# Optimization experiments

Hardware: AMD Instinct MI355X
Metric: run time of the kernel (lower is better)

## Reference

```python
import jax, jax.numpy as jnp
import numpy as np

NEG_SLOPE = 0.2

def _gatv2_layer(x, src, tgt, Wl, Wr, att, bias, num_nodes, heads, ch):
    # x: [N, Fin]; src/tgt: [E] (self loops already included)
    xl = (x @ Wl).reshape(num_nodes, heads, ch)  # source transform [N,H,C]
    xr = (x @ Wr).reshape(num_nodes, heads, ch)  # target transform [N,H,C]
    m = xl[src] + xr[tgt]                        # [E,H,C]
    m = jnp.where(m > 0, m, NEG_SLOPE * m)       # LeakyReLU
    e = jnp.einsum('ehc,hc->eh', m, att)         # attention logits [E,H]
    # softmax over incoming edges of each target node (numerically stable)
    e_max = jax.ops.segment_max(e, tgt, num_segments=num_nodes)
    e_max = jnp.where(jnp.isfinite(e_max), e_max, 0.0)
    alpha = jnp.exp(e - e_max[tgt])              # [E,H]
    denom = jax.ops.segment_sum(alpha, tgt, num_segments=num_nodes)
    alpha = alpha / (denom[tgt] + 1e-16)
    out = jax.ops.segment_sum(alpha[:, :, None] * xl[src], tgt, num_segments=num_nodes)  # [N,H,C]
    return out.mean(axis=1) + bias               # concat=False -> mean over heads, then bias


def setup_inputs() -> dict:
    key = jax.random.key(0)
    ks = jax.random.split(key, 12)
    N, E = 50000, 800000
    IN, HID, H = 128, 64, 2
    features = jax.random.normal(ks[0], (N, IN), dtype=jnp.float32)
    edge_index = jax.random.randint(ks[1], (2, E), 0, N, dtype=jnp.int64)
    s = 0.1
    return {
        'features': features,
        'edge_index': edge_index,
        'Wl1': jax.random.normal(ks[2], (IN, H * HID), dtype=jnp.float32) * s,
        'Wr1': jax.random.normal(ks[3], (IN, H * HID), dtype=jnp.float32) * s,
        'att1': jax.random.normal(ks[4], (H, HID), dtype=jnp.float32) * s,
        'b1': jnp.zeros((HID,), dtype=jnp.float32),
        'Wl2': jax.random.normal(ks[5], (HID, H * HID), dtype=jnp.float32) * s,
        'Wr2': jax.random.normal(ks[6], (HID, H * HID), dtype=jnp.float32) * s,
        'att2': jax.random.normal(ks[7], (H, HID), dtype=jnp.float32) * s,
        'b2': jnp.zeros((HID,), dtype=jnp.float32),
    }


def reference(features, edge_index, Wl1, Wr1, att1, b1, Wl2, Wr2, att2, b2):
    N = features.shape[0]
    H, HID = att1.shape
    # PyG GATv2Conv default add_self_loops=True
    loop = jnp.arange(N, dtype=edge_index.dtype)
    src = jnp.concatenate([edge_index[0], loop])
    tgt = jnp.concatenate([edge_index[1], loop])
    h = _gatv2_layer(features, src, tgt, Wl1, Wr1, att1, b1, N, H, HID)
    h = jax.nn.relu(h)
    out = _gatv2_layer(h, src, tgt, Wl2, Wr2, att2, b2, N, H, HID)
    return out  # node_mask in original is None
```

## Files before the change

kernel.cpp:

```cpp
#include <hip/hip_runtime.h>
#include <hip/hip_bf16.h>
#include <math.h>


#define HEADS 2
#define CH 64
#define FDIM (HEADS * CH)
#define CAP 48
#define HBLK 3328

typedef _Float16 f16_t;
typedef _Float16 f16x4 __attribute__((ext_vector_type(4)));
typedef _Float16 f16x8 __attribute__((ext_vector_type(8)));
typedef float f32x4 __attribute__((ext_vector_type(4)));


__global__ __launch_bounds__(256)
void init_kernel(const float* __restrict__ Wl1, const float* __restrict__ Wr1,
                 const float* __restrict__ Wl2, const float* __restrict__ Wr2,
                 f16_t* __restrict__ fl1, f16_t* __restrict__ fr1,
                 f16_t* __restrict__ fl2, f16_t* __restrict__ fr2,
                 int* __restrict__ cnt, int N) {
    int bx = blockIdx.x;
    if (bx < 4) {
        const float* W; f16_t* F; int K;
        switch (bx) {
            case 0:  W = Wl1; F = fl1; K = 128; break;
            case 1:  W = Wr1; F = fr1; K = 128; break;
            case 2:  W = Wl2; F = fl2; K = 64;  break;
            default: W = Wr2; F = fr2; K = 64;  break;
        }
        int S = K >> 5;
        int total = 8 * S * 64;
        for (int idx = threadIdx.x; idx < total; idx += blockDim.x) {
            int l  = idx & 63;
            int ts = idx >> 6;
            int s  = ts % S;
            int t  = ts / S;
            int n  = t * 16 + (l & 15);
            int k0 = s * 32 + (l >> 4) * 8;
            f16x8 v;
            #pragma unroll
            for (int j = 0; j < 8; ++j) v[j] = (f16_t)W[(size_t)(k0 + j) * 128 + n];
            *(f16x8*)(F + (size_t)idx * 8) = v;
        }
    } else {
        int n4 = (N + 3) >> 2;
        int stride = (gridDim.x - 4) * blockDim.x;
        for (int i = (bx - 4) * blockDim.x + threadIdx.x; i < n4; i += stride) {
            int i0 = i * 4;
            if (i0 + 3 < N) *(int4*)(cnt + i0) = make_int4(0, 0, 0, 0);
            else for (int k = 0; k < 4 && i0 + k < N; ++k) cnt[i0 + k] = 0;
        }
    }
}


__device__ __forceinline__ unsigned int pack_bf16x2(float x, float y) {
    __hip_bfloat16 lo = __float2bfloat16(x);
    __hip_bfloat16 hi = __float2bfloat16(y);
    unsigned short ulo = *reinterpret_cast<unsigned short*>(&lo);
    unsigned short uhi = *reinterpret_cast<unsigned short*>(&hi);
    return ((unsigned int)uhi << 16) | ulo;
}

__device__ __forceinline__
void gemm_body(const float* __restrict__ X,
               const f16_t* __restrict__ FL, const f16_t* __restrict__ FR,
               unsigned int* __restrict__ Y0b, float* __restrict__ Y1,
               int N, int K, int gblk, float* lds_f) {
    f16_t* Af = (f16_t*)lds_f;
    int tid  = threadIdx.x;
    int lane = tid & 63;
    int wave = tid >> 6;
    int row0 = gblk * 32;
    int S = K >> 5;

    {
        int r  = tid >> 3;
        int m  = r & 15;
        int g  = r >> 4;
        int gr = row0 + r;
        int kc = (tid & 7) * (K >> 3);
        const float* xp = X + (size_t)gr * K + kc;
        f16_t* areg = Af + g * (16 * K);
        for (int c = 0; c < (K >> 3); c += 4) {
            float4 xv = make_float4(0.f, 0.f, 0.f, 0.f);
            if (gr < N) xv = *(const float4*)(xp + c);
            int k = kc + c;
            int s = k >> 5;
            int lanei = ((k >> 3) & 3) * 16 + m;
            int j = k & 7;
            f16x4 h;
            h[0] = (f16_t)xv.x; h[1] = (f16_t)xv.y;
            h[2] = (f16_t)xv.z; h[3] = (f16_t)xv.w;
            *(f16x4*)(areg + ((s * 64 + lanei) * 8 + j)) = h;
        }
    }
    __syncthreads();

    int rg  = wave >> 1;
    int mat = wave & 1;
    const f16_t* F = mat ? FR : FL;

    f32x4 acc[8];
    #pragma unroll
    for (int t = 0; t < 8; ++t) acc[t] = (f32x4){0.f, 0.f, 0.f, 0.f};

    const f16_t* aw = Af + rg * (16 * K);
    for (int s = 0; s < S; ++s) {
        f16x8 a = *(const f16x8*)(aw + (s * 64 + lane) * 8);
        #pragma unroll
        for (int t = 0; t < 8; ++t) {
            f16x8 b = *(const f16x8*)(F + ((size_t)(t * S + s) * 64 + lane) * 8);
            acc[t] = __builtin_amdgcn_mfma_f32_16x16x32_f16(a, b, acc[t], 0, 0, 0);
        }
    }
    __syncthreads();

    float* ew = lds_f + wave * (16 * 68);
    int mrow = (lane >> 4) * 4;
    int ccol = lane & 15;
    int rr = lane & 15;
    int ch = lane >> 4;
    int gr2 = row0 + rg * 16 + rr;

    #pragma unroll
    for (int h = 0; h < 2; ++h) {
        #pragma unroll
        for (int tt = 0; tt < 4; ++tt)
            #pragma unroll
            for (int r = 0; r < 4; ++r)
                ew[(mrow + r) * 68 + tt * 16 + ccol] = acc[h * 4 + tt][r];
        __syncthreads();
        if (gr2 < N) {
            const float* src = ew + rr * 68 + ch * 16;
            if (mat == 0) {
                uint4 o0, o1;
                o0.x = pack_bf16x2(src[0],  src[1]);
                o0.y = pack_bf16x2(src[2],  src[3]);
                o0.z = pack_bf16x2(src[4],  src[5]);
                o0.w = pack_bf16x2(src[6],  src[7]);
                o1.x = pack_bf16x2(src[8],  src[9]);
                o1.y = pack_bf16x2(src[10], src[11]);
                o1.z = pack_bf16x2(src[12], src[13]);
                o1.w = pack_bf16x2(src[14], src[15]);
                unsigned int* dst = Y0b + (size_t)gr2 * (FDIM / 2) + h * 32 + ch * 8;
                *(uint4*)dst       = o0;
                *(uint4*)(dst + 4) = o1;
            } else {
                float* dst = Y1 + (size_t)gr2 * FDIM + h * 64 + ch * 16;
                #pragma unroll
                for (int q = 0; q < 4; ++q)
                    *(float4*)(dst + q * 4) = *(const float4*)(src + q * 4);
            }
        }
        __syncthreads();
    }
}

__global__ __launch_bounds__(256)
void fused_scatter_gemm_kernel(const float* __restrict__ X,
                               const f16_t* __restrict__ FL,
                               const f16_t* __restrict__ FR,
                               unsigned int* __restrict__ Y0b,
                               float* __restrict__ Y1,
                               int N, int K,
                               const int* __restrict__ ei, int* __restrict__ cnt,
                               int* __restrict__ ssrc, int E) {
    __shared__ float lds_f[4352];

    if (blockIdx.x < HBLK) {
        int vb   = blockIdx.x;
        int part = vb & 7;
        int blk  = vb >> 3;
        int nblk = HBLK >> 3;
        int lo = (int)(((long long)N * part) >> 3);
        int hi = (int)(((long long)N * (part + 1)) >> 3);
        int stride = nblk * blockDim.x;
        int G = E >> 2;
        for (int g = blk * blockDim.x + threadIdx.x; g < G; g += stride) {
            int4 t4 = *(const int4*)(ei + E + g * 4);
            if (t4.x >= lo && t4.x < hi) {
                int k = atomicAdd(&cnt[t4.x], 1);
                if (k < CAP) ssrc[t4.x * CAP + k] = ei[g * 4 + 0];
            }
            if (t4.y >= lo && t4.y < hi) {
                int k = atomicAdd(&cnt[t4.y], 1);
                if (k < CAP) ssrc[t4.y * CAP + k] = ei[g * 4 + 1];
            }
            if (t4.z >= lo && t4.z < hi) {
                int k = atomicAdd(&cnt[t4.z], 1);
                if (k < CAP) ssrc[t4.z * CAP + k] = ei[g * 4 + 2];
            }
            if (t4.w >= lo && t4.w < hi) {
                int k = atomicAdd(&cnt[t4.w], 1);
                if (k < CAP) ssrc[t4.w * CAP + k] = ei[g * 4 + 3];
            }
        }
        for (int e = (G << 2) + blk * blockDim.x + threadIdx.x; e < E; e += stride) {
            int t = ei[E + e];
            if (t >= lo && t < hi) {
                int k = atomicAdd(&cnt[t], 1);
                if (k < CAP) ssrc[t * CAP + k] = ei[e];
            }
        }
        for (int n = lo + blk * blockDim.x + threadIdx.x; n < hi; n += stride) {
            int k = atomicAdd(&cnt[n], 1);
            if (k < CAP) ssrc[n * CAP + k] = n;
        }
        return;
    }

    gemm_body(X, FL, FR, Y0b, Y1, N, K, blockIdx.x - HBLK, lds_f);
}

__global__ __launch_bounds__(256)
void gemm_kernel(const float* __restrict__ X,
                 const f16_t* __restrict__ FL, const f16_t* __restrict__ FR,
                 unsigned int* __restrict__ Y0b, float* __restrict__ Y1,
                 int N, int K) {
    __shared__ float lds_f[4352];
    gemm_body(X, FL, FR, Y0b, Y1, N, K, blockIdx.x, lds_f);
}


__device__ __forceinline__ void unpack_bf16x2(unsigned int u, float& x, float& y) {
    x = __uint_as_float(u << 16);
    y = __uint_as_float(u & 0xFFFF0000u);
}

__device__ __forceinline__ float2 lrelu2(float2 t) {
    t.x = fmaxf(t.x, 0.2f * t.x);
    t.y = fmaxf(t.y, 0.2f * t.y);
    return t;
}

__global__ __launch_bounds__(256)
void agg_kernel(const unsigned int* __restrict__ xlb, const float* __restrict__ xr,
                const int* __restrict__ cnt, const int* __restrict__ ssrc,
                const float* __restrict__ att, const float* __restrict__ bias,
                float* __restrict__ out, int N, int do_relu) {
    int node = blockIdx.x * 4 + (threadIdx.x >> 6);
    int lane = threadIdx.x & 63;
    if (node >= N) return;

    float2 xr2 = *(const float2*)(xr + (size_t)node * FDIM + 2 * lane);
    float2 a2  = *(const float2*)(att + 2 * lane);

    int beg = node * CAP;
    int deg = cnt[node];
    deg = min(deg, CAP);
    int end = beg + deg;

    float l = 0.f;
    float2 acc = make_float2(0.f, 0.f);

    bool b0 = (lane & 1) != 0;
    bool b1 = (lane & 2) != 0;
    bool b2 = (lane & 4) != 0;
    int base = lane & 32;

    int i = beg;
    int n8 = beg + (deg & ~7);
    for (; i < n8; i += 8) {
        int s0 = ssrc[i + 0];
        int s1 = ssrc[i + 1];
        int s2 = ssrc[i + 2];
        int s3 = ssrc[i + 3];
        int s4 = ssrc[i + 4];
        int s5 = ssrc[i + 5];
        int s6 = ssrc[i + 6];
        int s7 = ssrc[i + 7];
        unsigned int u0 = xlb[(size_t)s0 * (FDIM / 2) + lane];
        unsigned int u1 = xlb[(size_t)s1 * (FDIM / 2) + lane];
        unsigned int u2 = xlb[(size_t)s2 * (FDIM / 2) + lane];
        unsigned int u3 = xlb[(size_t)s3 * (FDIM / 2) + lane];
        unsigned int u4 = xlb[(size_t)s4 * (FDIM / 2) + lane];
        unsigned int u5 = xlb[(size_t)s5 * (FDIM / 2) + lane];
        unsigned int u6 = xlb[(size_t)s6 * (FDIM / 2) + lane];
        unsigned int u7 = xlb[(size_t)s7 * (FDIM / 2) + lane];
        float2 v0, v1, v2, v3, v4, v5, v6, v7;
        unpack_bf16x2(u0, v0.x, v0.y);
        unpack_bf16x2(u1, v1.x, v1.y);
        unpack_bf16x2(u2, v2.x, v2.y);
        unpack_bf16x2(u3, v3.x, v3.y);
        unpack_bf16x2(u4, v4.x, v4.y);
        unpack_bf16x2(u5, v5.x, v5.y);
        unpack_bf16x2(u6, v6.x, v6.y);
        unpack_bf16x2(u7, v7.x, v7.y);

        float2 t0 = lrelu2(make_float2(v0.x + xr2.x, v0.y + xr2.y));
        float2 t1 = lrelu2(make_float2(v1.x + xr2.x, v1.y + xr2.y));
        float2 t2 = lrelu2(make_float2(v2.x + xr2.x, v2.y + xr2.y));
        float2 t3 = lrelu2(make_float2(v3.x + xr2.x, v3.y + xr2.y));
        float2 t4 = lrelu2(make_float2(v4.x + xr2.x, v4.y + xr2.y));
        float2 t5 = lrelu2(make_float2(v5.x + xr2.x, v5.y + xr2.y));
        float2 t6 = lrelu2(make_float2(v6.x + xr2.x, v6.y + xr2.y));
        float2 t7 = lrelu2(make_float2(v7.x + xr2.x, v7.y + xr2.y));
        float p0 = fmaf(t0.x, a2.x, t0.y * a2.y);
        float p1 = fmaf(t1.x, a2.x, t1.y * a2.y);
        float p2 = fmaf(t2.x, a2.x, t2.y * a2.y);
        float p3 = fmaf(t3.x, a2.x, t3.y * a2.y);
        float p4 = fmaf(t4.x, a2.x, t4.y * a2.y);
        float p5 = fmaf(t5.x, a2.x, t5.y * a2.y);
        float p6 = fmaf(t6.x, a2.x, t6.y * a2.y);
        float p7 = fmaf(t7.x, a2.x, t7.y * a2.y);

        float s01 = (b0 ? p1 : p0) + __shfl_xor(b0 ? p0 : p1, 1, 64);
        float s23 = (b0 ? p3 : p2) + __shfl_xor(b0 ? p2 : p3, 1, 64);
        float s45 = (b0 ? p5 : p4) + __shfl_xor(b0 ? p4 : p5, 1, 64);
        float s67 = (b0 ? p7 : p6) + __shfl_xor(b0 ? p6 : p7, 1, 64);
        float q03 = (b1 ? s23 : s01) + __shfl_xor(b1 ? s01 : s23, 2, 64);
        float q47 = (b1 ? s67 : s45) + __shfl_xor(b1 ? s45 : s67, 2, 64);
        float r = (b2 ? q47 : q03) + __shfl_xor(b2 ? q03 : q47, 4, 64);
        r += __shfl_xor(r, 8, 64);
        r += __shfl_xor(r, 16, 64);

        float a = __expf(r);
        float al0 = __shfl(a, base | 0, 64);
        float al1 = __shfl(a, base | 1, 64);
        float al2 = __shfl(a, base | 2, 64);
        float al3 = __shfl(a, base | 3, 64);
        float al4 = __shfl(a, base | 4, 64);
        float al5 = __shfl(a, base | 5, 64);
        float al6 = __shfl(a, base | 6, 64);
        float al7 = __shfl(a, base | 7, 64);

        acc.x = fmaf(al0, v0.x, acc.x); acc.y = fmaf(al0, v0.y, acc.y);
        acc.x = fmaf(al1, v1.x, acc.x); acc.y = fmaf(al1, v1.y, acc.y);
        acc.x = fmaf(al2, v2.x, acc.x); acc.y = fmaf(al2, v2.y, acc.y);
        acc.x = fmaf(al3, v3.x, acc.x); acc.y = fmaf(al3, v3.y, acc.y);
        acc.x = fmaf(al4, v4.x, acc.x); acc.y = fmaf(al4, v4.y, acc.y);
        acc.x = fmaf(al5, v5.x, acc.x); acc.y = fmaf(al5, v5.y, acc.y);
        acc.x = fmaf(al6, v6.x, acc.x); acc.y = fmaf(al6, v6.y, acc.y);
        acc.x = fmaf(al7, v7.x, acc.x); acc.y = fmaf(al7, v7.y, acc.y);
        l += ((al0 + al1) + (al2 + al3)) + ((al4 + al5) + (al6 + al7));
    }
    int n4 = i + ((end - i) & ~3);
    for (; i < n4; i += 4) {
        int s0 = ssrc[i + 0];
        int s1 = ssrc[i + 1];
        int s2 = ssrc[i + 2];
        int s3 = ssrc[i + 3];
        unsigned int u0 = xlb[(size_t)s0 * (FDIM / 2) + lane];
        unsigned int u1 = xlb[(size_t)s1 * (FDIM / 2) + lane];
        unsigned int u2 = xlb[(size_t)s2 * (FDIM / 2) + lane];
        unsigned int u3 = xlb[(size_t)s3 * (FDIM / 2) + lane];
        float2 v0, v1, v2, v3;
        unpack_bf16x2(u0, v0.x, v0.y);
        unpack_bf16x2(u1, v1.x, v1.y);
        unpack_bf16x2(u2, v2.x, v2.y);
        unpack_bf16x2(u3, v3.x, v3.y);

        float2 t0 = lrelu2(make_float2(v0.x + xr2.x, v0.y + xr2.y));
        float2 t1 = lrelu2(make_float2(v1.x + xr2.x, v1.y + xr2.y));
        float2 t2 = lrelu2(make_float2(v2.x + xr2.x, v2.y + xr2.y));
        float2 t3 = lrelu2(make_float2(v3.x + xr2.x, v3.y + xr2.y));
        float p0 = fmaf(t0.x, a2.x, t0.y * a2.y);
        float p1 = fmaf(t1.x, a2.x, t1.y * a2.y);
        float p2 = fmaf(t2.x, a2.x, t2.y * a2.y);
        float p3 = fmaf(t3.x, a2.x, t3.y * a2.y);

        float s01 = (b0 ? p1 : p0) + __shfl_xor(b0 ? p0 : p1, 1, 64);
        float s23 = (b0 ? p3 : p2) + __shfl_xor(b0 ? p2 : p3, 1, 64);
        float q = (b1 ? s23 : s01) + __shfl_xor(b1 ? s01 : s23, 2, 64);
        q += __shfl_xor(q, 4, 64);
        q += __shfl_xor(q, 8, 64);
        q += __shfl_xor(q, 16, 64);
        float a = __expf(q);
        float al0 = __shfl(a, base | 0, 64);
        float al1 = __shfl(a, base | 1, 64);
        float al2 = __shfl(a, base | 2, 64);
        float al3 = __shfl(a, base | 3, 64);

        acc.x = fmaf(al0, v0.x, acc.x); acc.y = fmaf(al0, v0.y, acc.y);
        acc.x = fmaf(al1, v1.x, acc.x); acc.y = fmaf(al1, v1.y, acc.y);
        acc.x = fmaf(al2, v2.x, acc.x); acc.y = fmaf(al2, v2.y, acc.y);
        acc.x = fmaf(al3, v3.x, acc.x); acc.y = fmaf(al3, v3.y, acc.y);
        l += (al0 + al1) + (al2 + al3);
    }
    for (; i < end; ++i) {
        int s = ssrc[i];
        unsigned int u = xlb[(size_t)s * (FDIM / 2) + lane];
        float2 v;
        unpack_bf16x2(u, v.x, v.y);
        float2 t = lrelu2(make_float2(v.x + xr2.x, v.y + xr2.y));
        float p = fmaf(t.x, a2.x, t.y * a2.y);
        #pragma unroll
        for (int d = 1; d < 32; d <<= 1) p += __shfl_xor(p, d, 64);
        float al = __expf(p);
        acc.x = fmaf(al, v.x, acc.x);
        acc.y = fmaf(al, v.y, acc.y);
        l += al;
    }

    float inv = 1.0f / (l + 1e-16f);
    float rx = acc.x * inv;
    float ry = acc.y * inv;
    float ox = 0.5f * (rx + __shfl_xor(rx, 32, 64));
    float oy = 0.5f * (ry + __shfl_xor(ry, 32, 64));
    if (lane < 32) {
        float2 b = *(const float2*)(bias + 2 * lane);
        ox += b.x; oy += b.y;
        if (do_relu) { ox = fmaxf(ox, 0.f); oy = fmaxf(oy, 0.f); }
        *(float2*)(out + (size_t)node * CH + 2 * lane) = make_float2(ox, oy);
    }
}


static inline size_t align_up(size_t x, size_t a) { return (x + a - 1) & ~(a - 1); }

extern "C" void kernel_launch(void* const* d_in, const int* in_sizes, int n_in,
                              void* d_out, int out_size, void* d_ws, size_t ws_size,
                              hipStream_t stream) {
    const float* features = (const float*)d_in[0];
    const int*   ei       = (const int*)d_in[1];
    const float* Wl1      = (const float*)d_in[2];
    const float* Wr1      = (const float*)d_in[3];
    const float* att1     = (const float*)d_in[4];
    const float* b1       = (const float*)d_in[5];
    const float* Wl2      = (const float*)d_in[6];
    const float* Wr2      = (const float*)d_in[7];
    const float* att2     = (const float*)d_in[8];
    const float* b2       = (const float*)d_in[9];

    int N = in_sizes[0] / FDIM;
    int E = in_sizes[1] / 2;

    char* w = (char*)d_ws;
    int* cnt      = (int*)w;  w += align_up((size_t)N * 4, 256);
    int* ssrc     = (int*)w;  w += align_up((size_t)N * CAP * 4, 256);
    unsigned int* xlb = (unsigned int*)w; w += align_up((size_t)N * (FDIM / 2) * 4, 256);
    float* xr     = (float*)w; w += align_up((size_t)N * FDIM * 4, 256);
    float* hbuf   = (float*)w; w += align_up((size_t)N * CH * 4, 256);
    f16_t* fl1    = (f16_t*)w; w += align_up((size_t)8 * 4 * 64 * 8 * 2, 256);
    f16_t* fr1    = (f16_t*)w; w += align_up((size_t)8 * 4 * 64 * 8 * 2, 256);
    f16_t* fl2    = (f16_t*)w; w += align_up((size_t)8 * 2 * 64 * 8 * 2, 256);
    f16_t* fr2    = (f16_t*)w; w += align_up((size_t)8 * 2 * 64 * 8 * 2, 256);

    int gblocks = (N + 31) / 32;
    dim3 agrid((N + 3) / 4);

    init_kernel<<<56, 256, 0, stream>>>(Wl1, Wr1, Wl2, Wr2,
                                        fl1, fr1, fl2, fr2, cnt, N);

    fused_scatter_gemm_kernel<<<HBLK + gblocks, 256, 0, stream>>>(
        features, fl1, fr1, xlb, xr, N, 128, ei, cnt, ssrc, E);
    agg_kernel<<<agrid, 256, 0, stream>>>(xlb, xr, cnt, ssrc, att1, b1, hbuf, N, 1);

    gemm_kernel<<<gblocks, 256, 0, stream>>>(hbuf, fl2, fr2, xlb, xr, N, 64);
    agg_kernel<<<agrid, 256, 0, stream>>>(xlb, xr, cnt, ssrc, att2, b2, (float*)d_out, N, 0);
}
```

Measured before the change: 256.1 us.

## Emit layer-1 output as fp16 MFMA fragments and feed layer-2 GEMM directly

The first aggregation kernel now writes its ReLU output in fp16, stored directly in the MFMA A-operand fragment layout, instead of an fp32 row-major buffer. A new layer-2 GEMM kernel loads these fragments straight into registers, skipping the fp32 load, conversion and LDS staging that the generic GEMM body performed. This halves the intermediate buffer traffic and removes the staging work, at the cost of fp16 rounding of the hidden activations and a layout tied to 32-row blocks.

```diff
diff --git a/kernel.cpp b/kernel.cpp
--- a/kernel.cpp
+++ b/kernel.cpp
@@ -10,6 +10,7 @@
 #define HBLK 3328
 
 typedef _Float16 f16_t;
+typedef _Float16 f16x2 __attribute__((ext_vector_type(2)));
 typedef _Float16 f16x4 __attribute__((ext_vector_type(4)));
 typedef _Float16 f16x8 __attribute__((ext_vector_type(8)));
 typedef float f32x4 __attribute__((ext_vector_type(4)));
@@ -215,13 +216,79 @@
     gemm_body(X, FL, FR, Y0b, Y1, N, K, blockIdx.x - HBLK, lds_f);
 }
 
+
 __global__ __launch_bounds__(256)
-void gemm_kernel(const float* __restrict__ X,
-                 const f16_t* __restrict__ FL, const f16_t* __restrict__ FR,
-                 unsigned int* __restrict__ Y0b, float* __restrict__ Y1,
-                 int N, int K) {
+void gemm2pre_kernel(const f16_t* __restrict__ hfrag,
+                     const f16_t* __restrict__ FL, const f16_t* __restrict__ FR,
+                     unsigned int* __restrict__ Y0b, float* __restrict__ Y1,
+                     int N) {
     __shared__ float lds_f[4352];
-    gemm_body(X, FL, FR, Y0b, Y1, N, K, blockIdx.x, lds_f);
+    const int K = 64, S = 2;
+
+    int tid  = threadIdx.x;
+    int lane = tid & 63;
+    int wave = tid >> 6;
+    int gblk = blockIdx.x;
+    int row0 = gblk * 32;
+
+    int rg  = wave >> 1;
+    int mat = wave & 1;
+    const f16_t* F = mat ? FR : FL;
+
+    f32x4 acc[8];
+    #pragma unroll
+    for (int t = 0; t < 8; ++t) acc[t] = (f32x4){0.f, 0.f, 0.f, 0.f};
+
+    const f16_t* aw = hfrag + (size_t)gblk * (32 * K) + rg * (16 * K);
+    #pragma unroll
+    for (int s = 0; s < S; ++s) {
+        f16x8 a = *(const f16x8*)(aw + (s * 64 + lane) * 8);
+        #pragma unroll
+        for (int t = 0; t < 8; ++t) {
+            f16x8 b = *(const f16x8*)(F + ((size_t)(t * S + s) * 64 + lane) * 8);
+            acc[t] = __builtin_amdgcn_mfma_f32_16x16x32_f16(a, b, acc[t], 0, 0, 0);
+        }
+    }
+
+    float* ew = lds_f + wave * (16 * 68);
+    int mrow = (lane >> 4) * 4;
+    int ccol = lane & 15;
+    int rr = lane & 15;
+    int ch = lane >> 4;
+    int gr2 = row0 + rg * 16 + rr;
+
+    #pragma unroll
+    for (int h = 0; h < 2; ++h) {
+        #pragma unroll
+        for (int tt = 0; tt < 4; ++tt)
+            #pragma unroll
+            for (int r = 0; r < 4; ++r)
+                ew[(mrow + r) * 68 + tt * 16 + ccol] = acc[h * 4 + tt][r];
+        __syncthreads();
+        if (gr2 < N) {
+            const float* src = ew + rr * 68 + ch * 16;
+            if (mat == 0) {
+                uint4 o0, o1;
+                o0.x = pack_bf16x2(src[0],  src[1]);
+                o0.y = pack_bf16x2(src[2],  src[3]);
+                o0.z = pack_bf16x2(src[4],  src[5]);
+                o0.w = pack_bf16x2(src[6],  src[7]);
+                o1.x = pack_bf16x2(src[8],  src[9]);
+                o1.y = pack_bf16x2(src[10], src[11]);
+                o1.z = pack_bf16x2(src[12], src[13]);
+                o1.w = pack_bf16x2(src[14], src[15]);
+                unsigned int* dst = Y0b + (size_t)gr2 * (FDIM / 2) + h * 32 + ch * 8;
+                *(uint4*)dst       = o0;
+                *(uint4*)(dst + 4) = o1;
+            } else {
+                float* dst = Y1 + (size_t)gr2 * FDIM + h * 64 + ch * 16;
+                #pragma unroll
+                for (int q = 0; q < 4; ++q)
+                    *(float4*)(dst + q * 4) = *(const float4*)(src + q * 4);
+            }
+        }
+        __syncthreads();
+    }
 }
 
 
@@ -236,17 +303,11 @@
     return t;
 }
 
-__global__ __launch_bounds__(256)
-void agg_kernel(const unsigned int* __restrict__ xlb, const float* __restrict__ xr,
+__device__ __forceinline__
+float2 agg_core(const unsigned int* __restrict__ xlb, const float* __restrict__ xr,
                 const int* __restrict__ cnt, const int* __restrict__ ssrc,
-                const float* __restrict__ att, const float* __restrict__ bias,
-                float* __restrict__ out, int N, int do_relu) {
-    int node = blockIdx.x * 4 + (threadIdx.x >> 6);
-    int lane = threadIdx.x & 63;
-    if (node >= N) return;
-
+                float2 a2, int node, int lane) {
     float2 xr2 = *(const float2*)(xr + (size_t)node * FDIM + 2 * lane);
-    float2 a2  = *(const float2*)(att + 2 * lane);
 
     int beg = node * CAP;
     int deg = cnt[node];
@@ -396,15 +457,59 @@
     }
 
     float inv = 1.0f / (l + 1e-16f);
-    float rx = acc.x * inv;
-    float ry = acc.y * inv;
-    float ox = 0.5f * (rx + __shfl_xor(rx, 32, 64));
-    float oy = 0.5f * (ry + __shfl_xor(ry, 32, 64));
+    return make_float2(acc.x * inv, acc.y * inv);
+}
+
+__global__ __launch_bounds__(256)
+void agg_out_kernel(const unsigned int* __restrict__ xlb, const float* __restrict__ xr,
+                    const int* __restrict__ cnt, const int* __restrict__ ssrc,
+                    const float* __restrict__ att, const float* __restrict__ bias,
+                    float* __restrict__ out, int N, int do_relu) {
+    int node = blockIdx.x * 4 + (threadIdx.x >> 6);
+    int lane = threadIdx.x & 63;
+    if (node >= N) return;
+
+    float2 a2 = *(const float2*)(att + 2 * lane);
+    float2 r = agg_core(xlb, xr, cnt, ssrc, a2, node, lane);
+    float ox = 0.5f * (r.x + __shfl_xor(r.x, 32, 64));
+    float oy = 0.5f * (r.y + __shfl_xor(r.y, 32, 64));
     if (lane < 32) {
         float2 b = *(const float2*)(bias + 2 * lane);
         ox += b.x; oy += b.y;
         if (do_relu) { ox = fmaxf(ox, 0.f); oy = fmaxf(oy, 0.f); }
         *(float2*)(out + (size_t)node * CH + 2 * lane) = make_float2(ox, oy);
+    }
+}
+
+__global__ __launch_bounds__(256)
+void agg_frag_kernel(const unsigned int* __restrict__ xlb, const float* __restrict__ xr,
+                     const int* __restrict__ cnt, const int* __restrict__ ssrc,
+                     const float* __restrict__ att, const float* __restrict__ bias,
+                     f16_t* __restrict__ hfrag, int N) {
+    int node = blockIdx.x * 4 + (threadIdx.x >> 6);
+    int lane = threadIdx.x & 63;
+    if (node >= N) return;
+
+    float2 a2 = *(const float2*)(att + 2 * lane);
+    float2 r = agg_core(xlb, xr, cnt, ssrc, a2, node, lane);
+    float ox = 0.5f * (r.x + __shfl_xor(r.x, 32, 64));
+    float oy = 0.5f * (r.y + __shfl_xor(r.y, 32, 64));
+    if (lane < 32) {
+        float2 b = *(const float2*)(bias + 2 * lane);
+        ox = fmaxf(ox + b.x, 0.f);
+        oy = fmaxf(oy + b.y, 0.f);
+        int blk = node >> 5;
+        int g   = (node >> 4) & 1;
+        int m   = node & 15;
+        int k   = 2 * lane;
+        int s   = k >> 5;
+        int lanei = ((k >> 3) & 3) * 16 + m;
+        int j   = k & 7;
+        size_t off = (size_t)blk * 2048 + g * 1024 + (s * 64 + lanei) * 8 + j;
+        f16x2 hv;
+        hv[0] = (f16_t)ox;
+        hv[1] = (f16_t)oy;
+        *(f16x2*)(hfrag + off) = hv;
     }
 }
 
@@ -428,18 +533,19 @@
     int N = in_sizes[0] / FDIM;
     int E = in_sizes[1] / 2;
 
+    int gblocks = (N + 31) / 32;
+
     char* w = (char*)d_ws;
     int* cnt      = (int*)w;  w += align_up((size_t)N * 4, 256);
     int* ssrc     = (int*)w;  w += align_up((size_t)N * CAP * 4, 256);
     unsigned int* xlb = (unsigned int*)w; w += align_up((size_t)N * (FDIM / 2) * 4, 256);
     float* xr     = (float*)w; w += align_up((size_t)N * FDIM * 4, 256);
-    float* hbuf   = (float*)w; w += align_up((size_t)N * CH * 4, 256);
+    f16_t* hfrag  = (f16_t*)w; w += align_up((size_t)gblocks * 32 * 64 * 2, 256);
     f16_t* fl1    = (f16_t*)w; w += align_up((size_t)8 * 4 * 64 * 8 * 2, 256);
     f16_t* fr1    = (f16_t*)w; w += align_up((size_t)8 * 4 * 64 * 8 * 2, 256);
     f16_t* fl2    = (f16_t*)w; w += align_up((size_t)8 * 2 * 64 * 8 * 2, 256);
     f16_t* fr2    = (f16_t*)w; w += align_up((size_t)8 * 2 * 64 * 8 * 2, 256);
 
-    int gblocks = (N + 31) / 32;
     dim3 agrid((N + 3) / 4);
 
     init_kernel<<<56, 256, 0, stream>>>(Wl1, Wr1, Wl2, Wr2,
@@ -447,8 +553,10 @@
 
     fused_scatter_gemm_kernel<<<HBLK + gblocks, 256, 0, stream>>>(
         features, fl1, fr1, xlb, xr, N, 128, ei, cnt, ssrc, E);
-    agg_kernel<<<agrid, 256, 0, stream>>>(xlb, xr, cnt, ssrc, att1, b1, hbuf, N, 1);
-
-    gemm_kernel<<<gblocks, 256, 0, stream>>>(hbuf, fl2, fr2, xlb, xr, N, 64);
-    agg_kernel<<<agrid, 256, 0, stream>>>(xlb, xr, cnt, ssrc, att2, b2, (float*)d_out, N, 0);
-}
+    agg_frag_kernel<<<agrid, 256, 0, stream>>>(
+        xlb, xr, cnt, ssrc, att1, b1, hfrag, N);
+
+    gemm2pre_kernel<<<gblocks, 256, 0, stream>>>(hfrag, fl2, fr2, xlb, xr, N);
+    agg_out_kernel<<<agrid, 256, 0, stream>>>(
+        xlb, xr, cnt, ssrc, att2, b2, (float*)d_out, N, 0);
+}
```

Result: no change. 255.7 us (-0.2%).
